# Optimization experiments

Hardware: AMD Instinct MI355X
Metric: run time of the kernel (lower is better)

## Reference

```python
import jax, jax.numpy as jnp
import numpy as np

B, MAXN, F, H, T, L = 32, 1024, 215, 256, 8, 3
N = B * MAXN            # 32768 global nodes
E = 524288              # total edges, global indices


def setup_inputs() -> dict:
    key = jax.random.key(0)
    ks = jax.random.split(key, 12)
    s = 0.05
    return {
        "node_features": jax.random.normal(ks[0], (B, MAXN, F), dtype=jnp.float32),
        "edge_index": jax.random.randint(ks[1], (2, E), 0, N, dtype=jnp.int32),
        "edge_type": jax.random.randint(ks[2], (E,), 0, T, dtype=jnp.int32),
        # input projection
        "Wp": jax.random.normal(ks[3], (H, F), dtype=jnp.float32) * s,
        "bp": jax.random.normal(ks[4], (H,), dtype=jnp.float32) * s,
        # per-layer, per-edge-type message linears
        "Wm": jax.random.normal(ks[5], (L, T, H, H), dtype=jnp.float32) * s,
        "bm": jax.random.normal(ks[6], (L, T, H), dtype=jnp.float32) * s,
        # per-layer GRUCell params (torch layout: [r|z|n] stacked, 3H rows)
        "Wih": jax.random.normal(ks[7], (L, 3 * H, H), dtype=jnp.float32) * s,
        "Whh": jax.random.normal(ks[8], (L, 3 * H, H), dtype=jnp.float32) * s,
        "bih": jax.random.normal(ks[9], (L, 3 * H), dtype=jnp.float32) * s,
        "bhh": jax.random.normal(ks[10], (L, 3 * H), dtype=jnp.float32) * s,
    }


def _gru_cell(x, h, Wih, Whh, bih, bhh):
    # torch.nn.GRUCell math
    gi = x @ Wih.T + bih            # (N, 3H)
    gh = h @ Whh.T + bhh            # (N, 3H)
    i_r, i_z, i_n = jnp.split(gi, 3, axis=-1)
    h_r, h_z, h_n = jnp.split(gh, 3, axis=-1)
    r = jax.nn.sigmoid(i_r + h_r)
    z = jax.nn.sigmoid(i_z + h_z)
    n = jnp.tanh(i_n + r * h_n)
    return (1.0 - z) * n + z * h


def reference(node_features, edge_index, edge_type, Wp, bp, Wm, bm, Wih, Whh, bih, bhh):
    # flatten batch of graphs into global node array, project to hidden
    h = node_features.reshape(-1, F) @ Wp.T + bp          # (N, H)
    src, dst = edge_index[0], edge_index[1]
    for l in range(L):
        # apply all T type-specific linears to every node once (equivalent to
        # the per-edge-type mask+gather+Linear loop), then gather per edge
        Ht = jnp.einsum('nd,ted->nte', h, Wm[l]) + bm[l]  # (N, T, H)
        msg = Ht[src, edge_type]                           # (E, H) gather
        m = jax.ops.segment_sum(msg, dst, num_segments=N)  # scatter-add (N, H)
        h = _gru_cell(m, h, Wih[l], Whh[l], bih[l], bhh[l])
        # dropout is identity in eval mode
    # readout: full graphs -> sum each graph's node block
    return h.reshape(B, MAXN, H).sum(axis=1)               # (B, H)
```

## Files before the change

### kernel.cpp

```cpp
#include <hip/hip_runtime.h>

#define N_NODES 32768
#define E_EDGES 524288
#define F_IN    215
#define H_DIM   256
#define T_TYPES 8
#define L_LAYERS 3
#define B_GRAPHS 32
#define MAXN_   1024
#define NT_BINS (N_NODES * T_TYPES)

typedef float  f32x4  __attribute__((ext_vector_type(4)));
typedef __bf16 bf16x8 __attribute__((ext_vector_type(8)));

__device__ __forceinline__ unsigned short f2bf(float f) {
  union { float f; unsigned u; } v; v.f = f;
  unsigned r = v.u + 0x7fffu + ((v.u >> 16) & 1u);
  return (unsigned short)(r >> 16);
}
__device__ __forceinline__ float bf2f(unsigned short h) {
  union { unsigned u; float f; } v; v.u = ((unsigned)h) << 16;
  return v.f;
}
__device__ __forceinline__ float bflo(unsigned u) { union { unsigned x; float f; } v; v.x = u << 16; return v.f; }
__device__ __forceinline__ float bfhi(unsigned u) { union { unsigned x; float f; } v; v.x = u & 0xffff0000u; return v.f; }

typedef const __attribute__((address_space(1))) unsigned int* gas_ptr;
typedef __attribute__((address_space(3))) unsigned int* las_ptr;
__device__ __forceinline__ void gload_lds16(const unsigned short* g, unsigned short* l) {
  __builtin_amdgcn_global_load_lds((gas_ptr)g, (las_ptr)l, 16, 0, 0);
}

__device__ __forceinline__ void acc16(float* a, const uint4 v, const uint4 w) {
  a[0]  += bflo(v.x); a[1]  += bfhi(v.x);
  a[2]  += bflo(v.y); a[3]  += bfhi(v.y);
  a[4]  += bflo(v.z); a[5]  += bfhi(v.z);
  a[6]  += bflo(v.w); a[7]  += bfhi(v.w);
  a[8]  += bflo(w.x); a[9]  += bfhi(w.x);
  a[10] += bflo(w.y); a[11] += bfhi(w.y);
  a[12] += bflo(w.z); a[13] += bfhi(w.z);
  a[14] += bflo(w.w); a[15] += bfhi(w.w);
}

static constexpr size_t OFF_BIG     = 0;
static constexpr size_t REL_CURSOR  = 1048576;
static constexpr size_t REL_BSUM    = 2097152;
static constexpr size_t REL_WPPAD   = 33554432;
static constexpr size_t REL_HALT    = 50331648;
static constexpr size_t REL_OFFS    = 100663296;
static constexpr size_t REL_SORTED  = 104857600;
static constexpr size_t OFF_H_B     = 134217728;
static constexpr size_t OFF_M_B     = 150994944;
static constexpr size_t OFF_WMB     = 167772160;
static constexpr size_t OFF_WIH     = 170917888;
static constexpr size_t OFF_WHH     = 172097536;
static constexpr size_t WS_REQUIRED = 173277184;

__global__ void hist_kernel(const int* __restrict__ dst, const int* __restrict__ et,
                            int* __restrict__ cnt) {
  int e = blockIdx.x * 256 + threadIdx.x;
  atomicAdd(&cnt[dst[e] * T_TYPES + et[e]], 1);
}

__global__ __launch_bounds__(1024) void scan1(const int* __restrict__ cnt,
                                              int* __restrict__ offs,
                                              int* __restrict__ bsum) {
  __shared__ int wsum[16];
  const int t = threadIdx.x, lane = t & 63, wid = t >> 6;
  const int idx = blockIdx.x * 1024 + t;
  const int v = cnt[idx];
  int x = v;
  #pragma unroll
  for (int off = 1; off < 64; off <<= 1) {
    int u = __shfl_up(x, off, 64);
    if (lane >= off) x += u;
  }
  if (lane == 63) wsum[wid] = x;
  __syncthreads();
  int wbase = 0;
  for (int i = 0; i < wid; ++i) wbase += wsum[i];
  offs[idx] = wbase + x - v;
  if (t == 1023) bsum[blockIdx.x] = wbase + x;
}

__global__ __launch_bounds__(256) void scan2(int* __restrict__ bsum) {
  __shared__ int wsum[4];
  const int t = threadIdx.x, lane = t & 63, wid = t >> 6;
  const int v = bsum[t];
  int x = v;
  #pragma unroll
  for (int off = 1; off < 64; off <<= 1) {
    int u = __shfl_up(x, off, 64);
    if (lane >= off) x += u;
  }
  if (lane == 63) wsum[wid] = x;
  __syncthreads();
  int wbase = 0;
  for (int i = 0; i < wid; ++i) wbase += wsum[i];
  __syncthreads();
  bsum[t] = wbase + x - v;
}

__global__ __launch_bounds__(1024) void scan3(int* __restrict__ offs,
                                              const int* __restrict__ bsum,
                                              int* __restrict__ cursor) {
  const int idx = blockIdx.x * 1024 + threadIdx.x;
  const int o = offs[idx] + bsum[blockIdx.x];
  offs[idx] = o;
  cursor[idx] = o;
  if (idx == 0) offs[NT_BINS] = E_EDGES;
}

__global__ void reorder_kernel(const int* __restrict__ src, const int* __restrict__ dst,
                               const int* __restrict__ et, int* __restrict__ cursor,
                               unsigned short* __restrict__ sorted) {
  int e = blockIdx.x * 256 + threadIdx.x;
  int key = dst[e] * T_TYPES + et[e];
  int p = atomicAdd(&cursor[key], 1);
  sorted[p] = (unsigned short)src[e];
}

__global__ void cvt_weights(const float* __restrict__ a, const float* __restrict__ b,
                            const float* __restrict__ c,
                            unsigned short* __restrict__ oa, unsigned short* __restrict__ ob,
                            unsigned short* __restrict__ oc,
                            int na, int nb, int nc) {
  int i = blockIdx.x * 256 + threadIdx.x;
  if (i < na) { oa[i] = f2bf(a[i]); return; }
  int j = i - na;
  if (j < nb) { ob[j] = f2bf(b[j]); return; }
  int k = j - nb;
  if (k < nc) oc[k] = f2bf(c[k]);
}

__global__ void pad_cvt(const float* __restrict__ in, unsigned short* __restrict__ out,
                        int rows, int cin) {
  int i = blockIdx.x * 256 + threadIdx.x;
  if (i >= rows * 256) return;
  int r = i >> 8, c = i & 255;
  out[i] = (c < cin) ? f2bf(in[(size_t)r * cin + c]) : (unsigned short)0;
}

__global__ __launch_bounds__(256, 2) void gemm_bt(
    const unsigned short* __restrict__ A,
    const unsigned short* __restrict__ W,
    const float* __restrict__ bias,
    unsigned short* __restrict__ C,
    int M, int K) {
  __shared__ unsigned short As[2][128 * 32];
  __shared__ unsigned short Bs[2][128 * 32];
  const int tid = threadIdx.x;
  const int lane = tid & 63;
  const int wv = tid >> 6;
  const int lrow = lane & 15;
  const int lquad = lane >> 4;
  const int bm0 = blockIdx.x * 128;
  const int bn0 = blockIdx.y * 128;
  const int srow = wv * 16 + (lane >> 2);
  const int sslot = lane & 3;
  const int scol = sslot * 8;
  const int ssw = (sslot ^ ((lane >> 3) & 3)) * 8;
  const int rsw = (lquad ^ ((lane >> 1) & 3)) * 8;

  f32x4 acc[2][8] = {};

#define GBT_STAGE(b, kt)                                                              \
  { _Pragma("unroll") for (int i = 0; i < 2; ++i) {                                   \
      const int row = srow + i * 64;                                                  \
      gload_lds16(A + (size_t)(bm0 + row) * K + (kt) + ssw, &As[b][row * 32 + scol]); \
      gload_lds16(W + (size_t)(bn0 + row) * K + (kt) + ssw, &Bs[b][row * 32 + scol]); \
    } }

  GBT_STAGE(0, 0);
  __syncthreads();
  const int nk = K >> 5;
  for (int ki = 0; ki < nk; ++ki) {
    const int cur = ki & 1;
    if (ki + 1 < nk) GBT_STAGE(cur ^ 1, (ki + 1) * 32);
    bf16x8 af[2], bfr[8];
    #pragma unroll
    for (int mt = 0; mt < 2; ++mt)
      af[mt] = *(const bf16x8*)(&As[cur][(wv * 32 + mt * 16 + lrow) * 32 + rsw]);
    #pragma unroll
    for (int nt = 0; nt < 8; ++nt)
      bfr[nt] = *(const bf16x8*)(&Bs[cur][(nt * 16 + lrow) * 32 + rsw]);
    #pragma unroll
    for (int mt = 0; mt < 2; ++mt)
      #pragma unroll
      for (int nt = 0; nt < 8; ++nt)
        acc[mt][nt] = __builtin_amdgcn_mfma_f32_16x16x32_bf16(af[mt], bfr[nt], acc[mt][nt], 0, 0, 0);
    __syncthreads();
  }
#undef GBT_STAGE

  #pragma unroll
  for (int mt = 0; mt < 2; ++mt) {
    #pragma unroll
    for (int r = 0; r < 4; ++r) {
      const int grow = bm0 + wv * 32 + mt * 16 + lquad * 4 + r;
      #pragma unroll
      for (int nt = 0; nt < 8; ++nt) {
        const int gcol = bn0 + nt * 16 + lrow;
        float v = acc[mt][nt][r] + (bias ? bias[gcol] : 0.f);
        C[(size_t)grow * M + gcol] = f2bf(v);
      }
    }
  }
}

__global__ __launch_bounds__(512, 4) void msg_gemm(
    const int* __restrict__ offs, const unsigned short* __restrict__ sorted,
    const unsigned short* __restrict__ hb, const unsigned short* __restrict__ Wt_l,
    const float* __restrict__ bm_l, unsigned short* __restrict__ m) {
  constexpr int CH = 2568;
  __shared__ unsigned short Ss[8 * CH];
  __shared__ unsigned short Bs[2][256 * 32];
  __shared__ unsigned short idxS[2048];
  __shared__ int offsS[516];
  const int tid = threadIdx.x;
  const int lane = tid & 63;
  const int wv = tid >> 6;
  const int lrow = lane & 15;
  const int lquad = lane >> 4;
  const int wrow = wv & 3;
  const int wcol = wv >> 2;
  const int bm0 = blockIdx.x * 64;
  const int gg = wv * 4 + lquad;
  const int brow = tid >> 2;
  const int bslot = tid & 3;
  const int bcol = bslot * 8;
  const int bsw = (bslot ^ ((tid >> 3) & 3)) * 8;
  const int rsw = (lquad ^ ((lane >> 1) & 3)) * 8;

  const int gseg0 = offs[bm0 * 8];
  const int gseg1 = offs[bm0 * 8 + 512];
  const int seg = gseg1 - gseg0;
  for (int i = tid; i < 513; i += 512) offsS[i] = offs[bm0 * 8 + i];
  const int segc = seg < 2048 ? seg : 2048;
  for (int i = tid; i < segc; i += 512) idxS[i] = sorted[gseg0 + i];
  const bool useLds = (seg <= 2048);
  const unsigned short* ip = useLds ? (const unsigned short*)idxS : (sorted + gseg0);
  __syncthreads();

  f32x4 acc[8] = {};
  int buf = 0;

  for (int t = 0; t < T_TYPES; ++t) {
    #pragma unroll
    for (int step = 0; step < 2; ++step) {
      const int dloc = gg + step * 32;
      const int beg = offsS[dloc * 8 + t] - gseg0;
      const int end = offsS[dloc * 8 + t + 1] - gseg0;
      float a[16];
      #pragma unroll
      for (int j = 0; j < 16; ++j) a[j] = 0.f;
      int e = beg;
      if (e + 2 <= end) {
        int s0 = ip[e], s1 = ip[e + 1];
        const unsigned short* h0 = hb + (size_t)s0 * H_DIM + lrow * 16;
        const unsigned short* h1 = hb + (size_t)s1 * H_DIM + lrow * 16;
        uint4 pv0 = *(const uint4*)h0, pw0 = *(const uint4*)(h0 + 8);
        uint4 pv1 = *(const uint4*)h1, pw1 = *(const uint4*)(h1 + 8);
        e += 2;
        for (; e + 2 <= end; e += 2) {
          const int n0 = ip[e], n1 = ip[e + 1];
          const unsigned short* g0 = hb + (size_t)n0 * H_DIM + lrow * 16;
          const unsigned short* g1 = hb + (size_t)n1 * H_DIM + lrow * 16;
          const uint4 nv0 = *(const uint4*)g0, nw0 = *(const uint4*)(g0 + 8);
          const uint4 nv1 = *(const uint4*)g1, nw1 = *(const uint4*)(g1 + 8);
          acc16(a, pv0, pw0);
          acc16(a, pv1, pw1);
          pv0 = nv0; pw0 = nw0; pv1 = nv1; pw1 = nw1;
        }
        acc16(a, pv0, pw0);
        acc16(a, pv1, pw1);
      }
      if (e < end) {
        const int s0 = ip[e];
        const unsigned short* h0 = hb + (size_t)s0 * H_DIM + lrow * 16;
        acc16(a, *(const uint4*)h0, *(const uint4*)(h0 + 8));
      }
      union { unsigned short us[16]; uint4 q[2]; } ob;
      #pragma unroll
      for (int j = 0; j < 16; ++j) ob.us[j] = f2bf(a[j]);
      uint4* p = (uint4*)&Ss[(lrow >> 1) * CH + dloc * 40 + (lrow & 1) * 16];
      p[0] = ob.q[0];
      p[1] = ob.q[1];
    }
    const unsigned short* Wt = Wt_l + (size_t)t * 65536;
    gload_lds16(Wt + (size_t)brow * 256 + bsw, &Bs[buf][brow * 32 + bcol]);
    gload_lds16(Wt + (size_t)(brow + 128) * 256 + bsw, &Bs[buf][(brow + 128) * 32 + bcol]);
    __syncthreads();
    for (int kc = 0; kc < 8; ++kc) {
      if (kc < 7) {
        gload_lds16(Wt + (size_t)brow * 256 + (kc + 1) * 32 + bsw,
                    &Bs[buf ^ 1][brow * 32 + bcol]);
        gload_lds16(Wt + (size_t)(brow + 128) * 256 + (kc + 1) * 32 + bsw,
                    &Bs[buf ^ 1][(brow + 128) * 32 + bcol]);
      }
      const bf16x8 af = *(const bf16x8*)(&Ss[kc * CH + (wrow * 16 + lrow) * 40 + lquad * 8]);
      #pragma unroll
      for (int nt = 0; nt < 8; ++nt) {
        const bf16x8 b = *(const bf16x8*)(&Bs[buf][((wcol * 8 + nt) * 16 + lrow) * 32 + rsw]);
        acc[nt] = __builtin_amdgcn_mfma_f32_16x16x32_bf16(af, b, acc[nt], 0, 0, 0);
      }
      buf ^= 1;
      __syncthreads();
    }
  }

  float cnt[4][8];
  #pragma unroll
  for (int r = 0; r < 4; ++r) {
    const int dl = wrow * 16 + lquad * 4 + r;
    #pragma unroll
    for (int t = 0; t < 8; ++t)
      cnt[r][t] = (float)(offsS[dl * 8 + t + 1] - offsS[dl * 8 + t]);
  }
  #pragma unroll
  for (int nt = 0; nt < 8; ++nt) {
    const int gcol = wcol * 128 + nt * 16 + lrow;
    float bmv[8];
    #pragma unroll
    for (int t = 0; t < 8; ++t) bmv[t] = bm_l[t * H_DIM + gcol];
    #pragma unroll
    for (int r = 0; r < 4; ++r) {
      const int grow = bm0 + wrow * 16 + lquad * 4 + r;
      float v = acc[nt][r];
      #pragma unroll
      for (int t = 0; t < 8; ++t) v += cnt[r][t] * bmv[t];
      m[(size_t)grow * H_DIM + gcol] = f2bf(v);
    }
  }
}

__global__ __launch_bounds__(256, 2) void gru_fused(
    const unsigned short* __restrict__ mB,
    const unsigned short* __restrict__ hin,
    const unsigned short* __restrict__ wih_l,
    const unsigned short* __restrict__ whh_l,
    const float* __restrict__ bih_l,
    const float* __restrict__ bhh_l,
    unsigned short* __restrict__ hout) {
  __shared__ unsigned short Am[2][64 * 32];
  __shared__ unsigned short Ah[2][64 * 32];
  const int tid = threadIdx.x;
  const int lane = tid & 63;
  const int wv = tid >> 6;
  const int lrow = lane & 15;
  const int lquad = lane >> 4;
  const int n0 = blockIdx.x * 64;
  const int c0 = blockIdx.y * 64;
  const int arow = tid >> 2;
  const int sslot = tid & 3;
  const int ssw = (sslot ^ ((tid >> 3) & 3)) * 8;
  const int rsw = (lquad ^ ((lane >> 1) & 3)) * 8;
  const int wr = c0 + wv * 16 + lrow;

  f32x4 acc[6][4] = {};
  bf16x8 bfr[2][6];

#define GRU_LOADB(bi, kt)                                                                      \
  { _Pragma("unroll") for (int g = 0; g < 3; ++g) {                                            \
      bfr[bi][g]     = *(const bf16x8*)(wih_l + (size_t)(g * 256 + wr) * 256 + (kt) + lquad * 8); \
      bfr[bi][g + 3] = *(const bf16x8*)(whh_l + (size_t)(g * 256 + wr) * 256 + (kt) + lquad * 8); \
    } }
#define GRU_STAGE(b, kt)                                                                       \
  { gload_lds16(mB  + (size_t)(n0 + arow) * 256 + (kt) + ssw, &Am[b][arow * 32 + sslot * 8]);  \
    gload_lds16(hin + (size_t)(n0 + arow) * 256 + (kt) + ssw, &Ah[b][arow * 32 + sslot * 8]); }

  GRU_LOADB(0, 0);
  GRU_STAGE(0, 0);
  __syncthreads();

  #pragma unroll
  for (int ki = 0; ki < 8; ++ki) {
    const int cur = ki & 1;
    if (ki < 7) {
      GRU_LOADB(cur ^ 1, (ki + 1) * 32);
      GRU_STAGE(cur ^ 1, (ki + 1) * 32);
    }
    #pragma unroll
    for (int mt = 0; mt < 4; ++mt) {
      const bf16x8 am = *(const bf16x8*)(&Am[cur][(mt * 16 + lrow) * 32 + rsw]);
      const bf16x8 ah = *(const bf16x8*)(&Ah[cur][(mt * 16 + lrow) * 32 + rsw]);
      #pragma unroll
      for (int g = 0; g < 6; ++g)
        acc[g][mt] = __builtin_amdgcn_mfma_f32_16x16x32_bf16(g < 3 ? am : ah, bfr[cur][g], acc[g][mt], 0, 0, 0);
    }
    __syncthreads();
  }
#undef GRU_LOADB
#undef GRU_STAGE

  const int c = c0 + wv * 16 + lrow;
  const float b_ir = bih_l[c], b_iz = bih_l[256 + c], b_in = bih_l[512 + c];
  const float b_hr = bhh_l[c], b_hz = bhh_l[256 + c], b_hn = bhh_l[512 + c];
  #pragma unroll
  for (int mt = 0; mt < 4; ++mt) {
    #pragma unroll
    for (int r = 0; r < 4; ++r) {
      const int node = n0 + mt * 16 + lquad * 4 + r;
      const float i_r = acc[0][mt][r] + b_ir;
      const float i_z = acc[1][mt][r] + b_iz;
      const float i_n = acc[2][mt][r] + b_in;
      const float h_r = acc[3][mt][r] + b_hr;
      const float h_z = acc[4][mt][r] + b_hz;
      const float h_n = acc[5][mt][r] + b_hn;
      const float rr = 1.f / (1.f + __expf(-(i_r + h_r)));
      const float zz = 1.f / (1.f + __expf(-(i_z + h_z)));
      const float nn = tanhf(i_n + rr * h_n);
      const float hp = bf2f(hin[(size_t)node * 256 + c]);
      hout[(size_t)node * 256 + c] = f2bf((1.f - zz) * nn + zz * hp);
    }
  }
}

__global__ __launch_bounds__(256) void readout_partial(const unsigned short* __restrict__ hb,
                                                       float* __restrict__ part) {
  const int b = blockIdx.x >> 3;
  const int ch = blockIdx.x & 7;
  const int c = threadIdx.x;
  const unsigned short* base = hb + ((size_t)b * MAXN_ + ch * 128) * H_DIM + c;
  float s = 0.f;
  #pragma unroll 4
  for (int i = 0; i < 128; ++i) s += bf2f(base[(size_t)i * H_DIM]);
  part[(size_t)blockIdx.x * H_DIM + c] = s;
}

__global__ __launch_bounds__(256) void readout_final(const float* __restrict__ part,
                                                     float* __restrict__ out) {
  const int b = blockIdx.x;
  const int c = threadIdx.x;
  float s = 0.f;
  #pragma unroll
  for (int i = 0; i < 8; ++i) s += part[((size_t)b * 8 + i) * H_DIM + c];
  out[b * H_DIM + c] = s;
}

extern "C" void kernel_launch(void* const* d_in, const int* in_sizes, int n_in,
                              void* d_out, int out_size, void* d_ws, size_t ws_size,
                              hipStream_t stream) {
  if (ws_size < WS_REQUIRED) return;

  const float* X   = (const float*)d_in[0];
  const int*   ei  = (const int*)d_in[1];
  const int*   et  = (const int*)d_in[2];
  const float* Wp  = (const float*)d_in[3];
  const float* bp  = (const float*)d_in[4];
  const float* Wm  = (const float*)d_in[5];
  const float* bm  = (const float*)d_in[6];
  const float* Wih = (const float*)d_in[7];
  const float* Whh = (const float*)d_in[8];
  const float* bih = (const float*)d_in[9];
  const float* bhh = (const float*)d_in[10];
  float* out = (float*)d_out;
  char* ws = (char*)d_ws;

  int*            counts = (int*)(ws + OFF_BIG);
  int*            cursor = (int*)(ws + OFF_BIG + REL_CURSOR);
  int*            bsum   = (int*)(ws + OFF_BIG + REL_BSUM);
  unsigned short* xpad   = (unsigned short*)(ws + OFF_BIG);
  unsigned short* wppad  = (unsigned short*)(ws + OFF_BIG + REL_WPPAD);
  unsigned short* h_alt  = (unsigned short*)(ws + OFF_BIG + REL_HALT);
  float*          part   = (float*)(ws + OFF_BIG);
  int*            offs   = (int*)(ws + OFF_BIG + REL_OFFS);
  unsigned short* sorted = (unsigned short*)(ws + OFF_BIG + REL_SORTED);
  unsigned short* h_b    = (unsigned short*)(ws + OFF_H_B);
  unsigned short* m_b    = (unsigned short*)(ws + OFF_M_B);
  unsigned short* wmb    = (unsigned short*)(ws + OFF_WMB);
  unsigned short* wih_b  = (unsigned short*)(ws + OFF_WIH);
  unsigned short* whh_b  = (unsigned short*)(ws + OFF_WHH);

  const int* src = ei;
  const int* dst = ei + E_EDGES;

  hipMemsetAsync(counts, 0, NT_BINS * sizeof(int), stream);
  hist_kernel<<<E_EDGES / 256, 256, 0, stream>>>(dst, et, counts);
  scan1<<<NT_BINS / 1024, 1024, 0, stream>>>(counts, offs, bsum);
  scan2<<<1, 256, 0, stream>>>(bsum);
  scan3<<<NT_BINS / 1024, 1024, 0, stream>>>(offs, bsum, cursor);
  reorder_kernel<<<E_EDGES / 256, 256, 0, stream>>>(src, dst, et, cursor, sorted);

  pad_cvt<<<(N_NODES * 256) / 256, 256, 0, stream>>>(X, xpad, N_NODES, F_IN);
  pad_cvt<<<(256 * 256) / 256, 256, 0, stream>>>(Wp, wppad, 256, F_IN);
  {
    const int na = L_LAYERS * T_TYPES * H_DIM * H_DIM;
    const int nb = L_LAYERS * 3 * H_DIM * H_DIM;
    const int nc = nb;
    cvt_weights<<<(na + nb + nc + 255) / 256, 256, 0, stream>>>(
        Wm, Wih, Whh, wmb, wih_b, whh_b, na, nb, nc);
  }

  gemm_bt<<<dim3(N_NODES / 128, 2), 256, 0, stream>>>(xpad, wppad, bp, h_b, H_DIM, 256);

  for (int l = 0; l < L_LAYERS; ++l) {
    const unsigned short* wm_l  = wmb + (size_t)l * T_TYPES * H_DIM * H_DIM;
    const unsigned short* wih_l = wih_b + (size_t)l * 3 * H_DIM * H_DIM;
    const unsigned short* whh_l = whh_b + (size_t)l * 3 * H_DIM * H_DIM;
    const float* bm_l  = bm + (size_t)l * T_TYPES * H_DIM;
    const float* bih_l = bih + (size_t)l * 3 * H_DIM;
    const float* bhh_l = bhh + (size_t)l * 3 * H_DIM;

    unsigned short* h_cur = (l & 1) ? h_alt : h_b;
    unsigned short* h_nxt = (l & 1) ? h_b : h_alt;

    msg_gemm<<<N_NODES / 64, 512, 0, stream>>>(offs, sorted, h_cur, wm_l, bm_l, m_b);
    gru_fused<<<dim3(N_NODES / 64, 4), 256, 0, stream>>>(
        m_b, h_cur, wih_l, whh_l, bih_l, bhh_l, h_nxt);
  }

  readout_partial<<<B_GRAPHS * 8, 256, 0, stream>>>(h_alt, part);
  readout_final<<<B_GRAPHS, 256, 0, stream>>>(part, out);

  (void)in_sizes; (void)n_in; (void)out_size;
}
```

Before: 641.1 us.

## Pipeline weight loads with partial vmcnt waits in message and GRU kernels

In the message kernel, the first weight tile for the next edge type is prefetched during the last k-step of the current type, and the first tile is issued before the index setup. Full __syncthreads are replaced with raw s_barrier plus partial vmcnt waits so loads stay in flight across barriers. The GRU kernel moves to a triple-buffered LDS ring with a single barrier per k-step and vmcnt(8) waits. This targets exposed global-load latency and barrier stalls, but relies on hand-counted outstanding-load numbers, which are fragile if the compiler emits a different number of memory ops.

```diff
diff --git a/kernel.cpp b/kernel.cpp
--- a/kernel.cpp
+++ b/kernel.cpp
@@ -232,6 +232,12 @@
   const int bsw = (bslot ^ ((tid >> 3) & 3)) * 8;
   const int rsw = (lquad ^ ((lane >> 1) & 3)) * 8;
 
+#define MSG_STAGE(W_, kc_, b_)                                                         \
+  { gload_lds16((W_) + (size_t)brow * 256 + (kc_) * 32 + bsw, &Bs[b_][brow * 32 + bcol]); \
+    gload_lds16((W_) + (size_t)(brow + 128) * 256 + (kc_) * 32 + bsw,                  \
+                &Bs[b_][(brow + 128) * 32 + bcol]); }
+
+  MSG_STAGE(Wt_l, 0, 0);
   const int gseg0 = offs[bm0 * 8];
   const int gseg1 = offs[bm0 * 8 + 512];
   const int seg = gseg1 - gseg0;
@@ -287,17 +293,22 @@
       p[0] = ob.q[0];
       p[1] = ob.q[1];
     }
-    const unsigned short* Wt = Wt_l + (size_t)t * 65536;
-    gload_lds16(Wt + (size_t)brow * 256 + bsw, &Bs[buf][brow * 32 + bcol]);
-    gload_lds16(Wt + (size_t)(brow + 128) * 256 + bsw, &Bs[buf][(brow + 128) * 32 + bcol]);
     __syncthreads();
+    const unsigned short* Wt  = Wt_l + (size_t)t * 65536;
+    const unsigned short* Wtn = Wt_l + (size_t)(t + 1) * 65536;
     for (int kc = 0; kc < 8; ++kc) {
       if (kc < 7) {
-        gload_lds16(Wt + (size_t)brow * 256 + (kc + 1) * 32 + bsw,
-                    &Bs[buf ^ 1][brow * 32 + bcol]);
-        gload_lds16(Wt + (size_t)(brow + 128) * 256 + (kc + 1) * 32 + bsw,
-                    &Bs[buf ^ 1][(brow + 128) * 32 + bcol]);
+        MSG_STAGE(Wt, kc + 1, buf ^ 1);
+      } else if (t < 7) {
+        MSG_STAGE(Wtn, 0, buf ^ 1);
       }
+      if (t == 7 && kc == 7) {
+        asm volatile("s_waitcnt vmcnt(0)" ::: "memory");
+      } else {
+        asm volatile("s_waitcnt vmcnt(2)" ::: "memory");
+      }
+      __builtin_amdgcn_s_barrier();
+      __builtin_amdgcn_sched_barrier(0);
       const bf16x8 af = *(const bf16x8*)(&Ss[kc * CH + (wrow * 16 + lrow) * 40 + lquad * 8]);
       #pragma unroll
       for (int nt = 0; nt < 8; ++nt) {
@@ -305,9 +316,11 @@
         acc[nt] = __builtin_amdgcn_mfma_f32_16x16x32_bf16(af, b, acc[nt], 0, 0, 0);
       }
       buf ^= 1;
-      __syncthreads();
-    }
-  }
+      __builtin_amdgcn_s_barrier();
+      __builtin_amdgcn_sched_barrier(0);
+    }
+  }
+#undef MSG_STAGE
 
   float cnt[4][8];
   #pragma unroll
@@ -342,8 +355,8 @@
     const float* __restrict__ bih_l,
     const float* __restrict__ bhh_l,
     unsigned short* __restrict__ hout) {
-  __shared__ unsigned short Am[2][64 * 32];
-  __shared__ unsigned short Ah[2][64 * 32];
+  __shared__ unsigned short Am[3][64 * 32];
+  __shared__ unsigned short Ah[3][64 * 32];
   const int tid = threadIdx.x;
   const int lane = tid & 63;
   const int wv = tid >> 6;
@@ -371,24 +384,26 @@
 
   GRU_LOADB(0, 0);
   GRU_STAGE(0, 0);
-  __syncthreads();
 
   #pragma unroll
   for (int ki = 0; ki < 8; ++ki) {
-    const int cur = ki & 1;
     if (ki < 7) {
-      GRU_LOADB(cur ^ 1, (ki + 1) * 32);
-      GRU_STAGE(cur ^ 1, (ki + 1) * 32);
-    }
+      GRU_LOADB((ki + 1) & 1, (ki + 1) * 32);
+      GRU_STAGE((ki + 1) % 3, (ki + 1) * 32);
+      asm volatile("s_waitcnt vmcnt(8)" ::: "memory");
+    } else {
+      asm volatile("s_waitcnt vmcnt(0)" ::: "memory");
+    }
+    __builtin_amdgcn_s_barrier();
+    __builtin_amdgcn_sched_barrier(0);
     #pragma unroll
     for (int mt = 0; mt < 4; ++mt) {
-      const bf16x8 am = *(const bf16x8*)(&Am[cur][(mt * 16 + lrow) * 32 + rsw]);
-      const bf16x8 ah = *(const bf16x8*)(&Ah[cur][(mt * 16 + lrow) * 32 + rsw]);
+      const bf16x8 am = *(const bf16x8*)(&Am[ki % 3][(mt * 16 + lrow) * 32 + rsw]);
+      const bf16x8 ah = *(const bf16x8*)(&Ah[ki % 3][(mt * 16 + lrow) * 32 + rsw]);
       #pragma unroll
       for (int g = 0; g < 6; ++g)
-        acc[g][mt] = __builtin_amdgcn_mfma_f32_16x16x32_bf16(g < 3 ? am : ah, bfr[cur][g], acc[g][mt], 0, 0, 0);
-    }
-    __syncthreads();
+        acc[g][mt] = __builtin_amdgcn_mfma_f32_16x16x32_bf16(g < 3 ? am : ah, bfr[ki & 1][g], acc[g][mt], 0, 0, 0);
+    }
   }
 #undef GRU_LOADB
 #undef GRU_STAGE
```

After: 628.9 us. About the same (-1.9%).

## Read message weights directly from global memory instead of LDS double buffer

Applied to the files above, without the earlier changes.

Removes the LDS double-buffered staging of the per-type weight matrix in msg_gemm. Each wave now loads its own 32 output columns of B straight from global memory (through L2), and the MMA tiling changes so each wave covers all 64 rows with 4x2 tiles. This drops the LDS footprint and the per-k-chunk barriers, which may allow higher occupancy. The cost is more global/L2 traffic for weights with no prefetch overlap, and the latency of the direct loads can stall the MFMAs.

```diff
diff --git a/kernel.cpp b/kernel.cpp
--- a/kernel.cpp
+++ b/kernel.cpp
@@ -214,7 +214,6 @@
     const float* __restrict__ bm_l, unsigned short* __restrict__ m) {
   constexpr int CH = 2568;
   __shared__ unsigned short Ss[8 * CH];
-  __shared__ unsigned short Bs[2][256 * 32];
   __shared__ unsigned short idxS[2048];
   __shared__ int offsS[516];
   const int tid = threadIdx.x;
@@ -222,15 +221,8 @@
   const int wv = tid >> 6;
   const int lrow = lane & 15;
   const int lquad = lane >> 4;
-  const int wrow = wv & 3;
-  const int wcol = wv >> 2;
   const int bm0 = blockIdx.x * 64;
   const int gg = wv * 4 + lquad;
-  const int brow = tid >> 2;
-  const int bslot = tid & 3;
-  const int bcol = bslot * 8;
-  const int bsw = (bslot ^ ((tid >> 3) & 3)) * 8;
-  const int rsw = (lquad ^ ((lane >> 1) & 3)) * 8;
 
   const int gseg0 = offs[bm0 * 8];
   const int gseg1 = offs[bm0 * 8 + 512];
@@ -242,8 +234,7 @@
   const unsigned short* ip = useLds ? (const unsigned short*)idxS : (sorted + gseg0);
   __syncthreads();
 
-  f32x4 acc[8] = {};
-  int buf = 0;
+  f32x4 acc[2][4] = {};
 
   for (int t = 0; t < T_TYPES; ++t) {
     #pragma unroll
@@ -287,49 +278,50 @@
       p[0] = ob.q[0];
       p[1] = ob.q[1];
     }
+    __syncthreads();
     const unsigned short* Wt = Wt_l + (size_t)t * 65536;
-    gload_lds16(Wt + (size_t)brow * 256 + bsw, &Bs[buf][brow * 32 + bcol]);
-    gload_lds16(Wt + (size_t)(brow + 128) * 256 + bsw, &Bs[buf][(brow + 128) * 32 + bcol]);
+    #pragma unroll
+    for (int kc = 0; kc < 8; ++kc) {
+      bf16x8 af[4], bf[2];
+      #pragma unroll
+      for (int mt = 0; mt < 4; ++mt)
+        af[mt] = *(const bf16x8*)(&Ss[kc * CH + (mt * 16 + lrow) * 40 + lquad * 8]);
+      #pragma unroll
+      for (int ct = 0; ct < 2; ++ct)
+        bf[ct] = *(const bf16x8*)(Wt + (size_t)(wv * 32 + ct * 16 + lrow) * 256 + kc * 32 + lquad * 8);
+      #pragma unroll
+      for (int ct = 0; ct < 2; ++ct)
+        #pragma unroll
+        for (int mt = 0; mt < 4; ++mt)
+          acc[ct][mt] = __builtin_amdgcn_mfma_f32_16x16x32_bf16(af[mt], bf[ct], acc[ct][mt], 0, 0, 0);
+    }
     __syncthreads();
-    for (int kc = 0; kc < 8; ++kc) {
-      if (kc < 7) {
-        gload_lds16(Wt + (size_t)brow * 256 + (kc + 1) * 32 + bsw,
-                    &Bs[buf ^ 1][brow * 32 + bcol]);
-        gload_lds16(Wt + (size_t)(brow + 128) * 256 + (kc + 1) * 32 + bsw,
-                    &Bs[buf ^ 1][(brow + 128) * 32 + bcol]);
+  }
+
+  float bmv[2][8];
+  #pragma unroll
+  for (int ct = 0; ct < 2; ++ct) {
+    const int gcol = wv * 32 + ct * 16 + lrow;
+    #pragma unroll
+    for (int t = 0; t < 8; ++t) bmv[ct][t] = bm_l[t * H_DIM + gcol];
+  }
+  #pragma unroll
+  for (int mt = 0; mt < 4; ++mt) {
+    #pragma unroll
+    for (int r = 0; r < 4; ++r) {
+      const int dl = mt * 16 + lquad * 4 + r;
+      float c8[8];
+      #pragma unroll
+      for (int t = 0; t < 8; ++t)
+        c8[t] = (float)(offsS[dl * 8 + t + 1] - offsS[dl * 8 + t]);
+      #pragma unroll
+      for (int ct = 0; ct < 2; ++ct) {
+        const int gcol = wv * 32 + ct * 16 + lrow;
+        float v = acc[ct][mt][r];
+        #pragma unroll
+        for (int t = 0; t < 8; ++t) v += c8[t] * bmv[ct][t];
+        m[(size_t)(bm0 + dl) * H_DIM + gcol] = f2bf(v);
       }
-      const bf16x8 af = *(const bf16x8*)(&Ss[kc * CH + (wrow * 16 + lrow) * 40 + lquad * 8]);
-      #pragma unroll
-      for (int nt = 0; nt < 8; ++nt) {
-        const bf16x8 b = *(const bf16x8*)(&Bs[buf][((wcol * 8 + nt) * 16 + lrow) * 32 + rsw]);
-        acc[nt] = __builtin_amdgcn_mfma_f32_16x16x32_bf16(af, b, acc[nt], 0, 0, 0);
-      }
-      buf ^= 1;
-      __syncthreads();
-    }
-  }
-
-  float cnt[4][8];
-  #pragma unroll
-  for (int r = 0; r < 4; ++r) {
-    const int dl = wrow * 16 + lquad * 4 + r;
-    #pragma unroll
-    for (int t = 0; t < 8; ++t)
-      cnt[r][t] = (float)(offsS[dl * 8 + t + 1] - offsS[dl * 8 + t]);
-  }
-  #pragma unroll
-  for (int nt = 0; nt < 8; ++nt) {
-    const int gcol = wcol * 128 + nt * 16 + lrow;
-    float bmv[8];
-    #pragma unroll
-    for (int t = 0; t < 8; ++t) bmv[t] = bm_l[t * H_DIM + gcol];
-    #pragma unroll
-    for (int r = 0; r < 4; ++r) {
-      const int grow = bm0 + wrow * 16 + lquad * 4 + r;
-      float v = acc[nt][r];
-      #pragma unroll
-      for (int t = 0; t < 8; ++t) v += cnt[r][t] * bmv[t];
-      m[(size_t)grow * H_DIM + gcol] = f2bf(v);
     }
   }
 }
```

New measurement: 691.3 us. +7.8%, slower.
